# Kernel optimization log

Measured on AMD Instinct MI355X. Metric: run time of the kernel, lower is better.

The kernel has to match this reference:

```python
import jax, jax.numpy as jnp
import numpy as np

E, H, BLOCK = 1024, 64, 2048

def setup_inputs() -> dict:
    key = jax.random.key(0)
    kx, kk, kq, kv = jax.random.split(key, 4)
    s = 1.0 / np.sqrt(E)
    return {
        "x": jax.random.normal(kx, (16, 2048, E), dtype=jnp.float32),
        "Wk": jax.random.uniform(kk, (E, H), jnp.float32, -s, s),
        "Wq": jax.random.uniform(kq, (E, H), jnp.float32, -s, s),
        "Wv": jax.random.uniform(kv, (E, H), jnp.float32, -s, s),
    }

def reference(x, Wk, Wq, Wv):
    B, T, C = x.shape
    k = x @ Wk  # [B,T,H]
    q = x @ Wq
    v = x @ Wv
    scale = jnp.asarray(H, x.dtype) ** -0.5
    wei = jnp.einsum("bth,bsh->bts", q, k) * scale  # [B,T,T]
    causal = jnp.tril(jnp.ones((T, T), dtype=bool))
    wei = jnp.where(causal, wei, -jnp.inf)
    wei = jax.nn.softmax(wei, axis=-1)
    # dropout is identity in eval mode
    return jnp.einsum("bts,bsh->bth", wei, v)
```

## Files before the change

### kernel.cpp

```cpp
#include <hip/hip_runtime.h>


typedef __bf16 bf16x8 __attribute__((ext_vector_type(8)));
typedef __bf16 bf16x4 __attribute__((ext_vector_type(4)));
typedef float f32x4 __attribute__((ext_vector_type(4)));

constexpr int kE = 1024;
constexpr int kH = 64;
constexpr int kT = 2048;
constexpr int kB = 16;
constexpr int kM = kB * kT;
constexpr float kQScale = 0.125f * 1.44269504088896340736f;

#define MFMA16(a, b, c) __builtin_amdgcn_mfma_f32_16x16x32_bf16((a), (b), (c), 0, 0, 0)

__global__ __launch_bounds__(256)
void prep_w(const float* __restrict__ Wq, const float* __restrict__ Wk,
            const float* __restrict__ Wv, __bf16* __restrict__ WbT)
{
    __shared__ float tl[64][65];
    const int mat = blockIdx.x >> 4;
    const int k0 = (blockIdx.x & 15) * 64;
    const float* src = (mat == 0) ? Wq : (mat == 1) ? Wk : Wv;

    const int t = threadIdx.x;
    const int kr = t >> 2;
    const int cg = (t & 3) * 16;
    #pragma unroll
    for (int i = 0; i < 4; ++i) {
        float4 v = *(const float4*)&src[(size_t)(k0 + kr) * kH + cg + 4 * i];
        tl[cg + 4 * i + 0][kr] = v.x;
        tl[cg + 4 * i + 1][kr] = v.y;
        tl[cg + 4 * i + 2][kr] = v.z;
        tl[cg + 4 * i + 3][kr] = v.w;
    }
    __syncthreads();
    const int nl = t >> 2;
    const int kg = (t & 3) * 16;
    bf16x8 o0, o1;
    #pragma unroll
    for (int j = 0; j < 8; ++j) {
        o0[j] = (__bf16)tl[nl][kg + j];
        o1[j] = (__bf16)tl[nl][kg + 8 + j];
    }
    *(bf16x8*)&WbT[(size_t)(mat * 64 + nl) * kE + k0 + kg] = o0;
    *(bf16x8*)&WbT[(size_t)(mat * 64 + nl) * kE + k0 + kg + 8] = o1;
}

__global__ __launch_bounds__(256)
void qkv(const float* __restrict__ x, const __bf16* __restrict__ WbT,
         __bf16* __restrict__ qo, __bf16* __restrict__ ko, __bf16* __restrict__ vT)
{
    const int t = threadIdx.x;
    const int lane = t & 63;
    const int w = t >> 6;
    const int l15 = lane & 15;
    const int q = lane >> 4;
    const int row0 = blockIdx.x * 64;

    f32x4 acc[4][3];
    #pragma unroll
    for (int mt = 0; mt < 4; ++mt)
        #pragma unroll
        for (int nt = 0; nt < 3; ++nt) acc[mt][nt] = (f32x4){0.f, 0.f, 0.f, 0.f};

    const float* xrow[4];
    #pragma unroll
    for (int mt = 0; mt < 4; ++mt)
        xrow[mt] = &x[(size_t)(row0 + mt * 16 + l15) * kE + q * 8];
    const __bf16* brow[3];
    #pragma unroll
    for (int nt = 0; nt < 3; ++nt)
        brow[nt] = &WbT[(size_t)(w * 48 + nt * 16 + l15) * kE + q * 8];

    #pragma unroll 2
    for (int k0 = 0; k0 < kE; k0 += 64) {
        bf16x8 bfrag[2][3];
        #pragma unroll
        for (int ks = 0; ks < 2; ++ks)
            #pragma unroll
            for (int nt = 0; nt < 3; ++nt)
                bfrag[ks][nt] = *(const bf16x8*)&brow[nt][k0 + ks * 32];

        bf16x8 afrag[2][4];
        #pragma unroll
        for (int mt = 0; mt < 4; ++mt)
            #pragma unroll
            for (int ks = 0; ks < 2; ++ks) {
                float4 u0 = *(const float4*)&xrow[mt][k0 + ks * 32];
                float4 u1 = *(const float4*)&xrow[mt][k0 + ks * 32 + 4];
                bf16x8 a;
                a[0] = (__bf16)u0.x; a[1] = (__bf16)u0.y;
                a[2] = (__bf16)u0.z; a[3] = (__bf16)u0.w;
                a[4] = (__bf16)u1.x; a[5] = (__bf16)u1.y;
                a[6] = (__bf16)u1.z; a[7] = (__bf16)u1.w;
                afrag[ks][mt] = a;
            }

        #pragma unroll
        for (int ks = 0; ks < 2; ++ks)
            #pragma unroll
            for (int nt = 0; nt < 3; ++nt)
                #pragma unroll
                for (int mt = 0; mt < 4; ++mt)
                    acc[mt][nt] = MFMA16(afrag[ks][mt], bfrag[ks][nt], acc[mt][nt]);
    }

    const int batch = row0 >> 11;
    const int tr0 = row0 & 2047;
    #pragma unroll
    for (int nt = 0; nt < 3; ++nt) {
        const int col0 = w * 48 + nt * 16;
        const int mat = col0 >> 6;
        const int c = (col0 & 63) + l15;
        if (mat == 2) {
            #pragma unroll
            for (int mt = 0; mt < 4; ++mt) {
                const int trow = tr0 + mt * 16 + q * 4;
                bf16x4 pk;
                #pragma unroll
                for (int r = 0; r < 4; ++r) pk[r] = (__bf16)acc[mt][nt][r];
                *(bf16x4*)&vT[((size_t)batch * kH + c) * kT + trow] = pk;
            }
        } else {
            __bf16* dst = (mat == 0) ? qo : ko;
            const float sc_ = (mat == 0) ? kQScale : 1.0f;
            #pragma unroll
            for (int mt = 0; mt < 4; ++mt)
                #pragma unroll
                for (int r = 0; r < 4; ++r) {
                    const size_t row = row0 + mt * 16 + q * 4 + r;
                    dst[row * kH + c] = (__bf16)(acc[mt][nt][r] * sc_);
                }
        }
    }
}

__global__ __launch_bounds__(256)
void attn(const __bf16* __restrict__ qm, const __bf16* __restrict__ km,
          const __bf16* __restrict__ vT, float* __restrict__ out)
{
    __shared__ __align__(16) __bf16 Ks[64][72];
    __shared__ __align__(16) __bf16 Vt[64][72];
    __shared__ __align__(16) __bf16 Ps[4][16][72];

    const int t = threadIdx.x;
    const int lane = t & 63;
    const int w = t >> 6;
    const int l15 = lane & 15;
    const int Q = lane >> 4;

    const int batch = blockIdx.x & 15;
    const int qi = 31 - (blockIdx.x >> 4);
    const int q0 = qi * 64;
    const int qrow = q0 + w * 16 + l15;

    const __bf16* qb = qm + (size_t)batch * kT * kH;
    const __bf16* kb = km + (size_t)batch * kT * kH;
    const __bf16* vb = vT + (size_t)batch * kH * kT;

    bf16x8 aq[2];
    aq[0] = *(const bf16x8*)&qb[(size_t)qrow * kH + Q * 8];
    aq[1] = *(const bf16x8*)&qb[(size_t)qrow * kH + 32 + Q * 8];

    f32x4 O[4];
    #pragma unroll
    for (int i = 0; i < 4; ++i) O[i] = (f32x4){0.f, 0.f, 0.f, 0.f};
    float m_ = -3.0e38f, l_ = 0.f;

    const int sr = t >> 2;
    const int scg = (t & 3) * 16;

    bf16x8 k0r, k1r, v0r, v1r;
    {
        k0r = *(const bf16x8*)&kb[(size_t)sr * kH + scg];
        k1r = *(const bf16x8*)&kb[(size_t)sr * kH + scg + 8];
        v0r = *(const bf16x8*)&vb[(size_t)sr * kT + scg];
        v1r = *(const bf16x8*)&vb[(size_t)sr * kT + scg + 8];
    }

    for (int kt = 0; kt <= qi; ++kt) {
        *(bf16x8*)&Ks[sr][scg] = k0r;
        *(bf16x8*)&Ks[sr][scg + 8] = k1r;
        *(bf16x8*)&Vt[sr][scg] = v0r;
        *(bf16x8*)&Vt[sr][scg + 8] = v1r;
        __syncthreads();

        if (kt < qi) {
            const int sn = (kt + 1) * 64;
            k0r = *(const bf16x8*)&kb[(size_t)(sn + sr) * kH + scg];
            k1r = *(const bf16x8*)&kb[(size_t)(sn + sr) * kH + scg + 8];
            v0r = *(const bf16x8*)&vb[(size_t)sr * kT + sn + scg];
            v1r = *(const bf16x8*)&vb[(size_t)sr * kT + sn + scg + 8];
        }

        bf16x8 kf[8], vf[8];
        #pragma unroll
        for (int ks = 0; ks < 2; ++ks)
            #pragma unroll
            for (int nt = 0; nt < 4; ++nt)
                kf[ks * 4 + nt] = *(const bf16x8*)&Ks[nt * 16 + l15][ks * 32 + Q * 8];
        #pragma unroll
        for (int ht = 0; ht < 4; ++ht)
            #pragma unroll
            for (int ss = 0; ss < 2; ++ss)
                vf[ht * 2 + ss] = *(const bf16x8*)&Vt[ht * 16 + l15][ss * 32 + Q * 8];

        f32x4 sacc[4];
        #pragma unroll
        for (int nt = 0; nt < 4; ++nt) sacc[nt] = (f32x4){0.f, 0.f, 0.f, 0.f};
        #pragma unroll
        for (int ks = 0; ks < 2; ++ks)
            #pragma unroll
            for (int nt = 0; nt < 4; ++nt)
                sacc[nt] = MFMA16(kf[ks * 4 + nt], aq[ks], sacc[nt]);

        if (kt == qi) {
            const int s0 = kt * 64;
            #pragma unroll
            for (int nt = 0; nt < 4; ++nt)
                #pragma unroll
                for (int r = 0; r < 4; ++r)
                    if (s0 + nt * 16 + Q * 4 + r > qrow) sacc[nt][r] = -3.0e38f;
        }

        float mx = sacc[0][0];
        #pragma unroll
        for (int nt = 0; nt < 4; ++nt)
            #pragma unroll
            for (int r = 0; r < 4; ++r) mx = fmaxf(mx, sacc[nt][r]);
        mx = fmaxf(mx, __shfl_xor(mx, 16));
        mx = fmaxf(mx, __shfl_xor(mx, 32));
        const float mnew = fmaxf(m_, mx);
        const float alpha = __builtin_amdgcn_exp2f(m_ - mnew);
        float rs = 0.f;
        #pragma unroll
        for (int nt = 0; nt < 4; ++nt)
            #pragma unroll
            for (int r = 0; r < 4; ++r) {
                const float p = __builtin_amdgcn_exp2f(sacc[nt][r] - mnew);
                sacc[nt][r] = p;
                rs += p;
            }
        rs += __shfl_xor(rs, 16);
        rs += __shfl_xor(rs, 32);
        l_ = l_ * alpha + rs;
        m_ = mnew;
        #pragma unroll
        for (int ht = 0; ht < 4; ++ht) O[ht] *= alpha;

        #pragma unroll
        for (int nt = 0; nt < 4; ++nt) {
            bf16x4 pk;
            #pragma unroll
            for (int r = 0; r < 4; ++r) pk[r] = (__bf16)sacc[nt][r];
            *(bf16x4*)&Ps[w][l15][nt * 16 + Q * 4] = pk;
        }
        bf16x8 pb0 = *(const bf16x8*)&Ps[w][l15][Q * 8];
        bf16x8 pb1 = *(const bf16x8*)&Ps[w][l15][32 + Q * 8];

        #pragma unroll
        for (int ht = 0; ht < 4; ++ht) {
            O[ht] = MFMA16(vf[ht * 2 + 0], pb0, O[ht]);
            O[ht] = MFMA16(vf[ht * 2 + 1], pb1, O[ht]);
        }
        __syncthreads();
    }

    const float inv = 1.0f / l_;
    float* orow = out + ((size_t)batch * kT + qrow) * kH;
    #pragma unroll
    for (int ht = 0; ht < 4; ++ht) {
        float4 o4;
        o4.x = O[ht][0] * inv; o4.y = O[ht][1] * inv;
        o4.z = O[ht][2] * inv; o4.w = O[ht][3] * inv;
        *(float4*)&orow[ht * 16 + Q * 4] = o4;
    }
}

extern "C" void kernel_launch(void* const* d_in, const int* in_sizes, int n_in,
                              void* d_out, int out_size, void* d_ws, size_t ws_size,
                              hipStream_t stream)
{
    (void)in_sizes; (void)n_in; (void)out_size; (void)ws_size;
    const float* x  = (const float*)d_in[0];
    const float* Wk = (const float*)d_in[1];
    const float* Wq = (const float*)d_in[2];
    const float* Wv = (const float*)d_in[3];

    __bf16* WbT  = (__bf16*)d_ws;
    __bf16* qb   = WbT + (size_t)192 * kE;
    __bf16* kbuf = qb + (size_t)kM * kH;
    __bf16* vT   = kbuf + (size_t)kM * kH;

    prep_w<<<48, 256, 0, stream>>>(Wq, Wk, Wv, WbT);
    qkv<<<kM / 64, 256, 0, stream>>>(x, WbT, qb, kbuf, vT);
    attn<<<kB * 32, 256, 0, stream>>>(qb, kbuf, vT, (float*)d_out);
}
```

Before: 285.2 us.

## Double-buffer K/V shared tiles in attention and software-pipeline QKV loads

The attention kernel now keeps two shared-memory K/V buffers and writes the next tile into the spare buffer after the MFMAs, dropping one barrier per iteration. The QKV projection loop is restructured into explicit ping-pong register buffers so global loads for the next 64-wide k-slice are issued before the current slice is computed. Both kernels get launch_bounds(256,1), allowing more registers per thread at the cost of occupancy. The doubled LDS and higher register use may reduce how many blocks fit per CU.

Measured after the change: 278.0 us. 2.5% less time.

```diff
diff --git a/kernel.cpp b/kernel.cpp
--- a/kernel.cpp
+++ b/kernel.cpp
@@ -47,7 +47,7 @@
     *(bf16x8*)&WbT[(size_t)(mat * 64 + nl) * kE + k0 + kg + 8] = o1;
 }
 
-__global__ __launch_bounds__(256)
+__global__ __launch_bounds__(256, 1)
 void qkv(const float* __restrict__ x, const __bf16* __restrict__ WbT,
          __bf16* __restrict__ qo, __bf16* __restrict__ ko, __bf16* __restrict__ vT)
 {
@@ -73,37 +73,52 @@
     for (int nt = 0; nt < 3; ++nt)
         brow[nt] = &WbT[(size_t)(w * 48 + nt * 16 + l15) * kE + q * 8];
 
-    #pragma unroll 2
-    for (int k0 = 0; k0 < kE; k0 += 64) {
-        bf16x8 bfrag[2][3];
+    float4 A0[4][2][2], A1[4][2][2];
+    bf16x8 B0[2][3], B1[2][3];
+
+    auto load = [&](float4 (&A)[4][2][2], bf16x8 (&Bv)[2][3], int k0) {
+        #pragma unroll
+        for (int mt = 0; mt < 4; ++mt)
+            #pragma unroll
+            for (int ks = 0; ks < 2; ++ks) {
+                A[mt][ks][0] = *(const float4*)&xrow[mt][k0 + ks * 32];
+                A[mt][ks][1] = *(const float4*)&xrow[mt][k0 + ks * 32 + 4];
+            }
         #pragma unroll
         for (int ks = 0; ks < 2; ++ks)
             #pragma unroll
             for (int nt = 0; nt < 3; ++nt)
-                bfrag[ks][nt] = *(const bf16x8*)&brow[nt][k0 + ks * 32];
-
-        bf16x8 afrag[2][4];
-        #pragma unroll
-        for (int mt = 0; mt < 4; ++mt)
-            #pragma unroll
-            for (int ks = 0; ks < 2; ++ks) {
-                float4 u0 = *(const float4*)&xrow[mt][k0 + ks * 32];
-                float4 u1 = *(const float4*)&xrow[mt][k0 + ks * 32 + 4];
+                Bv[ks][nt] = *(const bf16x8*)&brow[nt][k0 + ks * 32];
+    };
+    auto compute = [&](float4 (&A)[4][2][2], bf16x8 (&Bv)[2][3]) {
+        #pragma unroll
+        for (int ks = 0; ks < 2; ++ks) {
+            bf16x8 af[4];
+            #pragma unroll
+            for (int mt = 0; mt < 4; ++mt) {
+                float4 u0 = A[mt][ks][0], u1 = A[mt][ks][1];
                 bf16x8 a;
                 a[0] = (__bf16)u0.x; a[1] = (__bf16)u0.y;
                 a[2] = (__bf16)u0.z; a[3] = (__bf16)u0.w;
                 a[4] = (__bf16)u1.x; a[5] = (__bf16)u1.y;
                 a[6] = (__bf16)u1.z; a[7] = (__bf16)u1.w;
-                afrag[ks][mt] = a;
+                af[mt] = a;
             }
-
-        #pragma unroll
-        for (int ks = 0; ks < 2; ++ks)
             #pragma unroll
             for (int nt = 0; nt < 3; ++nt)
                 #pragma unroll
                 for (int mt = 0; mt < 4; ++mt)
-                    acc[mt][nt] = MFMA16(afrag[ks][mt], bfrag[ks][nt], acc[mt][nt]);
+                    acc[mt][nt] = MFMA16(af[mt], Bv[ks][nt], acc[mt][nt]);
+        }
+    };
+
+    load(A0, B0, 0);
+    #pragma unroll 1
+    for (int k0 = 0; k0 < kE; k0 += 128) {
+        if (k0 + 64 < kE) load(A1, B1, k0 + 64);
+        compute(A0, B0);
+        if (k0 + 128 < kE) load(A0, B0, k0 + 128);
+        if (k0 + 64 < kE) compute(A1, B1);
     }
 
     const int batch = row0 >> 11;
@@ -136,12 +151,12 @@
     }
 }
 
-__global__ __launch_bounds__(256)
+__global__ __launch_bounds__(256, 1)
 void attn(const __bf16* __restrict__ qm, const __bf16* __restrict__ km,
           const __bf16* __restrict__ vT, float* __restrict__ out)
 {
-    __shared__ __align__(16) __bf16 Ks[64][72];
-    __shared__ __align__(16) __bf16 Vt[64][72];
+    __shared__ __align__(16) __bf16 Ks[2][64][72];
+    __shared__ __align__(16) __bf16 Vt[2][64][72];
     __shared__ __align__(16) __bf16 Ps[4][16][72];
 
     const int t = threadIdx.x;
@@ -172,20 +187,18 @@
     const int scg = (t & 3) * 16;
 
     bf16x8 k0r, k1r, v0r, v1r;
-    {
-        k0r = *(const bf16x8*)&kb[(size_t)sr * kH + scg];
-        k1r = *(const bf16x8*)&kb[(size_t)sr * kH + scg + 8];
-        v0r = *(const bf16x8*)&vb[(size_t)sr * kT + scg];
-        v1r = *(const bf16x8*)&vb[(size_t)sr * kT + scg + 8];
-    }
+    k0r = *(const bf16x8*)&kb[(size_t)sr * kH + scg];
+    k1r = *(const bf16x8*)&kb[(size_t)sr * kH + scg + 8];
+    v0r = *(const bf16x8*)&vb[(size_t)sr * kT + scg];
+    v1r = *(const bf16x8*)&vb[(size_t)sr * kT + scg + 8];
+    *(bf16x8*)&Ks[0][sr][scg] = k0r;
+    *(bf16x8*)&Ks[0][sr][scg + 8] = k1r;
+    *(bf16x8*)&Vt[0][sr][scg] = v0r;
+    *(bf16x8*)&Vt[0][sr][scg + 8] = v1r;
+    __syncthreads();
 
     for (int kt = 0; kt <= qi; ++kt) {
-        *(bf16x8*)&Ks[sr][scg] = k0r;
-        *(bf16x8*)&Ks[sr][scg + 8] = k1r;
-        *(bf16x8*)&Vt[sr][scg] = v0r;
-        *(bf16x8*)&Vt[sr][scg + 8] = v1r;
-        __syncthreads();
-
+        const int p = kt & 1;
         if (kt < qi) {
             const int sn = (kt + 1) * 64;
             k0r = *(const bf16x8*)&kb[(size_t)(sn + sr) * kH + scg];
@@ -199,12 +212,12 @@
         for (int ks = 0; ks < 2; ++ks)
             #pragma unroll
             for (int nt = 0; nt < 4; ++nt)
-                kf[ks * 4 + nt] = *(const bf16x8*)&Ks[nt * 16 + l15][ks * 32 + Q * 8];
+                kf[ks * 4 + nt] = *(const bf16x8*)&Ks[p][nt * 16 + l15][ks * 32 + Q * 8];
         #pragma unroll
         for (int ht = 0; ht < 4; ++ht)
             #pragma unroll
             for (int ss = 0; ss < 2; ++ss)
-                vf[ht * 2 + ss] = *(const bf16x8*)&Vt[ht * 16 + l15][ss * 32 + Q * 8];
+                vf[ht * 2 + ss] = *(const bf16x8*)&Vt[p][ht * 16 + l15][ss * 32 + Q * 8];
 
         f32x4 sacc[4];
         #pragma unroll
@@ -238,9 +251,9 @@
         for (int nt = 0; nt < 4; ++nt)
             #pragma unroll
             for (int r = 0; r < 4; ++r) {
-                const float p = __builtin_amdgcn_exp2f(sacc[nt][r] - mnew);
-                sacc[nt][r] = p;
-                rs += p;
+                const float p_ = __builtin_amdgcn_exp2f(sacc[nt][r] - mnew);
+                sacc[nt][r] = p_;
+                rs += p_;
             }
         rs += __shfl_xor(rs, 16);
         rs += __shfl_xor(rs, 32);
@@ -263,6 +276,13 @@
         for (int ht = 0; ht < 4; ++ht) {
             O[ht] = MFMA16(vf[ht * 2 + 0], pb0, O[ht]);
             O[ht] = MFMA16(vf[ht * 2 + 1], pb1, O[ht]);
+        }
+
+        if (kt < qi) {
+            *(bf16x8*)&Ks[1 - p][sr][scg] = k0r;
+            *(bf16x8*)&Ks[1 - p][sr][scg + 8] = k1r;
+            *(bf16x8*)&Vt[1 - p][sr][scg] = v0r;
+            *(bf16x8*)&Vt[1 - p][sr][scg + 8] = v1r;
         }
         __syncthreads();
     }
```
